# Kernel tuning notes

Hardware: AMD Instinct MI355X
Metric: run time of the kernel (lower is better)

## Reference

```python
import jax, jax.numpy as jnp
import numpy as np

N_NODES = 100000
N_EDGES = 1600000
D_IN = 128
D_HID = 128
N_CLASSES = 10
N_GRAPHS = 512


def setup_inputs() -> dict:
    key = jax.random.key(0)
    ks = jax.random.split(key, 12)
    x = jax.random.normal(ks[0], (N_NODES, D_IN), dtype=jnp.float32)
    edge_src = jax.random.randint(ks[1], (N_EDGES,), 0, N_NODES, dtype=jnp.int32)
    edge_dst = jax.random.randint(ks[2], (N_EDGES,), 0, N_NODES, dtype=jnp.int32)
    batch = jnp.sort(jax.random.randint(ks[3], (N_NODES,), 0, N_GRAPHS, dtype=jnp.int32))
    # GCNConv weights (glorot-ish scale) and biases
    def w(k, fi, fo):
        return jax.random.normal(k, (fi, fo), dtype=jnp.float32) / np.sqrt(fi)
    W0 = w(ks[4], D_IN, D_HID);  b0 = jnp.zeros((D_HID,), jnp.float32)
    W1 = w(ks[5], D_HID, D_HID); b1 = jnp.zeros((D_HID,), jnp.float32)
    W2 = w(ks[6], D_HID, D_HID); b2 = jnp.zeros((D_HID,), jnp.float32)
    Wc = w(ks[7], D_HID, N_CLASSES); bc = jnp.zeros((N_CLASSES,), jnp.float32)
    return {"x": x, "edge_src": edge_src, "edge_dst": edge_dst, "batch": batch,
            "W0": W0, "b0": b0, "W1": W1, "b1": b1, "W2": W2, "b2": b2,
            "Wc": Wc, "bc": bc}


def _gcn_conv(x, W, b, src, dst, dinv):
    # PyG GCNConv: h = x @ W; out[i] = sum_{j->i} dinv[j]*dinv[i]*h[j] (incl. self-loop) + b
    h = x @ W                                   # [N, F_out]
    norm = (dinv[src] * dinv[dst])[:, None]     # [E, 1]
    agg = jax.ops.segment_sum(h[src] * norm, dst, num_segments=N_NODES)
    agg = agg + h * (dinv * dinv)[:, None]      # self-loop contribution
    return agg + b


def reference(x, edge_src, edge_dst, batch, W0, b0, W1, b1, W2, b2, Wc, bc):
    # symmetric normalization: deg over dst with self-loops added
    deg = jax.ops.segment_sum(jnp.ones((N_EDGES,), jnp.float32), edge_dst,
                              num_segments=N_NODES) + 1.0
    dinv = jax.lax.rsqrt(deg)
    h = jax.nn.relu(_gcn_conv(x, W0, b0, edge_src, edge_dst, dinv))
    h = jax.nn.relu(_gcn_conv(h, W1, b1, edge_src, edge_dst, dinv))
    h = jax.nn.relu(_gcn_conv(h, W2, b2, edge_src, edge_dst, dinv))
    # global mean pool over graphs
    sums = jax.ops.segment_sum(h, batch, num_segments=N_GRAPHS)      # [G, D]
    cnts = jax.ops.segment_sum(jnp.ones((N_NODES,), jnp.float32), batch,
                               num_segments=N_GRAPHS)
    pooled = sums / jnp.maximum(cnts, 1.0)[:, None]
    return pooled @ Wc + bc                                          # [G, C]
```

## Files before the change

kernel.cpp:

```cpp
#include <hip/hip_runtime.h>

#define NN 100000
#define NE 1600000
#define DF 128
#define NG 512
#define NC 10
#define NBK 256
#define NPBN 391
#define BKCAP 8192
#define PCH 4096

typedef unsigned short u16;
typedef unsigned int u32;
typedef __bf16 bf16_t;
typedef bf16_t bf16x8 __attribute__((ext_vector_type(8)));
typedef float f32x4 __attribute__((ext_vector_type(4)));

__device__ __forceinline__ u16 f2bf(float f){
  u32 x=__float_as_uint(f);
  u32 r=(x+0x7fffu+((x>>16)&1u))>>16;
  return (u16)r;
}
__device__ __forceinline__ float bflo(u32 u){ return __uint_as_float(u<<16); }
__device__ __forceinline__ float bfhi(u32 u){ return __uint_as_float(u&0xffff0000u); }

__global__ void k_setup(int* __restrict__ cur,
                        const float* __restrict__ W0, const float* __restrict__ W1,
                        const float* __restrict__ W2, u16* __restrict__ WT,
                        const int* __restrict__ batch, int* __restrict__ goff){
  int i=blockIdx.x*256+threadIdx.x;
  if(i<NBK) cur[i]=0;
  if(i<3*DF*DF){
    int w=i>>14, r=i&16383;
    const float* W = (w==0)?W0:((w==1)?W1:W2);
    int k=r>>7, n=r&127;
    WT[(size_t)w*DF*DF + n*128+k]=f2bf(W[r]);
  }
  if(i<=NG){
    int lo=0, hi=NN;
    while(lo<hi){ int mid=(lo+hi)>>1; if(batch[mid]<i) lo=mid+1; else hi=mid; }
    goff[i]=lo;
  }
}

__global__ __launch_bounds__(256) void k_part(const int* __restrict__ esrc, const int* __restrict__ edst,
                                              int* __restrict__ cur, uint2* __restrict__ pairs, int n){
  __shared__ int hist[NBK], basev[NBK], lscan[NBK], lcur[NBK];
  __shared__ uint2 stage[PCH];
  int tid=threadIdx.x;
  int start=blockIdx.x*PCH, end=min(start+PCH,n);
  if(tid<NBK) hist[tid]=0;
  __syncthreads();
  for(int i=start+tid;i<end;i+=256) atomicAdd(&hist[(u32)edst[i]/NPBN],1);
  __syncthreads();
  if(tid<64){
    int carry=0;
    #pragma unroll
    for(int c=0;c<NBK;c+=64){
      int v=hist[c+tid], x=v;
      #pragma unroll
      for(int off=1;off<64;off<<=1){ int t=__shfl_up(x,off,64); if(tid>=off) x+=t; }
      lscan[c+tid]=x-v+carry;
      carry+=__shfl(x,63,64);
    }
  }
  __syncthreads();
  if(tid<NBK){ basev[tid]=atomicAdd(&cur[tid],hist[tid]); lcur[tid]=0; }
  __syncthreads();
  for(int i=start+tid;i<end;i+=256){
    int d=edst[i], s=esrc[i];
    int b=(u32)d/NPBN;
    int p=lscan[b]+atomicAdd(&lcur[b],1);
    stage[p]=make_uint2((u32)s,(u32)d);
  }
  __syncthreads();
  int ntot=end-start;
  for(int i=tid;i<ntot;i+=256){
    uint2 e=stage[i];
    int b=(u32)e.y/NPBN;
    pairs[(size_t)b*BKCAP + basev[b] + (i - lscan[b])]=e;
  }
}

__global__ __launch_bounds__(256) void k_bucket(const uint2* __restrict__ pairs, const int* __restrict__ cur,
                                                int* __restrict__ offs, float* __restrict__ dinv,
                                                int* __restrict__ csr){
  __shared__ int hist[NPBN], lsc[NPBN], curL[NBK];
  __shared__ int sbase[2];
  int b=blockIdx.x, tid=threadIdx.x;
  if(tid<NBK) curL[tid]=cur[tid];
  for(int j=tid;j<NPBN;j+=256) hist[j]=0;
  __syncthreads();
  if(tid<64){
    int acc=0;
    #pragma unroll
    for(int c=0;c<NBK;c+=64){
      int v=(c+tid<b)? curL[c+tid] : 0;
      #pragma unroll
      for(int off=32;off;off>>=1) v+=__shfl_xor(v,off,64);
      acc+=v;
    }
    if(tid==0){ sbase[0]=acc; sbase[1]=curL[b]; }
  }
  __syncthreads();
  int base=sbase[0], count=sbase[1];
  int node0=b*NPBN;
  int nnode=min(NPBN, NN-node0);
  const uint2* P=pairs+(size_t)b*BKCAP;
  for(int i=tid;i<count;i+=256) atomicAdd(&hist[P[i].y-node0],1);
  __syncthreads();
  if(tid<64){
    int carry=0;
    #pragma unroll
    for(int c=0;c<448;c+=64){
      int idx=c+tid;
      int v=(idx<NPBN)? hist[idx] : 0, x=v;
      #pragma unroll
      for(int off=1;off<64;off<<=1){ int t=__shfl_up(x,off,64); if(tid>=off) x+=t; }
      if(idx<NPBN) lsc[idx]=x-v+carry;
      carry+=__shfl(x,63,64);
    }
  }
  __syncthreads();
  for(int j=tid;j<nnode;j+=256){
    offs[node0+j]=base+lsc[j];
    dinv[node0+j]=rsqrtf((float)hist[j]+1.0f);
  }
  if(b==NBK-1 && tid==0) offs[NN]=base+count;
  __syncthreads();
  for(int j=tid;j<nnode;j+=256) hist[j]=lsc[j];
  __syncthreads();
  for(int i=tid;i<count;i+=256){
    uint2 e=P[i];
    int p=atomicAdd(&hist[e.y-node0],1);
    csr[base+p]=(int)e.x;
  }
}

template<bool F32IN>
__global__ __launch_bounds__(256) void k_gemm(const void* __restrict__ Ap, const u16* __restrict__ WT,
                                              const float* __restrict__ dinv, u16* __restrict__ outp, int n){
  __shared__ u16 sA[128][136];
  __shared__ u16 sW[128][136];
  int tid=threadIdx.x;
  int row0=blockIdx.x*128;
  {
    const uint4* p=(const uint4*)WT;
    #pragma unroll
    for(int j=0;j<8;++j){
      int c=tid+j*256;
      int r=c>>4, c8=c&15;
      *(uint4*)&sW[r][c8*8]=p[c];
    }
  }
  if(F32IN){
    const float4* A4=(const float4*)Ap;
    #pragma unroll
    for(int j=0;j<16;++j){
      int c=tid+j*256;
      int r=c>>5, c4=c&31;
      int row=row0+r;
      float4 v = (row<n)? A4[(size_t)row*32+c4] : make_float4(0.f,0.f,0.f,0.f);
      u32 lo=(u32)f2bf(v.x) | ((u32)f2bf(v.y)<<16);
      u32 hi=(u32)f2bf(v.z) | ((u32)f2bf(v.w)<<16);
      uint2 q; q.x=lo; q.y=hi;
      *(uint2*)&sA[r][c4*4]=q;
    }
  } else {
    const uint4* A4=(const uint4*)Ap;
    #pragma unroll
    for(int j=0;j<8;++j){
      int c=tid+j*256;
      int r=c>>4, c8=c&15;
      int row=row0+r;
      uint4 v = (row<n)? A4[(size_t)row*16+c8] : make_uint4(0,0,0,0);
      *(uint4*)&sA[r][c8*8]=v;
    }
  }
  __syncthreads();
  int wv=tid>>6, lane=tid&63;
  int lr=lane&15, lk=lane>>4;
  f32x4 acc[2][8];
  #pragma unroll
  for(int mr=0;mr<2;++mr)
    #pragma unroll
    for(int nt=0;nt<8;++nt) acc[mr][nt]=(f32x4){0.f,0.f,0.f,0.f};
  #pragma unroll
  for(int kk=0;kk<4;++kk){
    bf16x8 a[2], b[8];
    #pragma unroll
    for(int mr=0;mr<2;++mr)
      a[mr]=*(const bf16x8*)&sA[wv*32+mr*16+lr][kk*32+lk*8];
    #pragma unroll
    for(int nt=0;nt<8;++nt)
      b[nt]=*(const bf16x8*)&sW[nt*16+lr][kk*32+lk*8];
    #pragma unroll
    for(int mr=0;mr<2;++mr)
      #pragma unroll
      for(int nt=0;nt<8;++nt)
        acc[mr][nt]=__builtin_amdgcn_mfma_f32_16x16x32_bf16(a[mr],b[nt],acc[mr][nt],0,0,0);
  }
  #pragma unroll
  for(int mr=0;mr<2;++mr){
    int rbase=row0+wv*32+mr*16+lk*4;
    #pragma unroll
    for(int r=0;r<4;++r){
      int row=rbase+r;
      if(row<n){
        float di=dinv[row];
        #pragma unroll
        for(int nt=0;nt<8;++nt)
          outp[(size_t)row*128+nt*16+lr]=f2bf(acc[mr][nt][r]*di);
      }
    }
  }
}

__global__ __launch_bounds__(256) void k_agg(const u16* __restrict__ h2, const int* __restrict__ offs,
                                             const int* __restrict__ csr, const float* __restrict__ dinv,
                                             const float* __restrict__ bias, u16* __restrict__ outp, int n){
  int wid=threadIdx.x>>6, lane=threadIdx.x&63;
  int node=blockIdx.x*4+wid;
  if(node>=n) return;
  const u32* hv=(const u32*)h2;
  u32 sv=hv[(size_t)node*64+lane];
  float ax=bflo(sv), ay=bfhi(sv);
  int e=offs[node], e1=offs[node+1];
  for(; e+16<=e1; e+=16){
    int ii[16];
    #pragma unroll
    for(int j=0;j<16;++j) ii[j]=csr[e+j];
    u32 vv[16];
    #pragma unroll
    for(int j=0;j<16;++j) vv[j]=hv[(size_t)ii[j]*64+lane];
    #pragma unroll
    for(int j=0;j<16;++j){ ax+=bflo(vv[j]); ay+=bfhi(vv[j]); }
  }
  if(e+8<=e1){
    int ii[8];
    #pragma unroll
    for(int j=0;j<8;++j) ii[j]=csr[e+j];
    u32 vv[8];
    #pragma unroll
    for(int j=0;j<8;++j) vv[j]=hv[(size_t)ii[j]*64+lane];
    #pragma unroll
    for(int j=0;j<8;++j){ ax+=bflo(vv[j]); ay+=bfhi(vv[j]); }
    e+=8;
  }
  if(e+4<=e1){
    int i0=csr[e],i1=csr[e+1],i2=csr[e+2],i3=csr[e+3];
    u32 v0=hv[(size_t)i0*64+lane], v1=hv[(size_t)i1*64+lane];
    u32 v2=hv[(size_t)i2*64+lane], v3=hv[(size_t)i3*64+lane];
    ax+=bflo(v0)+bflo(v1)+bflo(v2)+bflo(v3);
    ay+=bfhi(v0)+bfhi(v1)+bfhi(v2)+bfhi(v3);
    e+=4;
  }
  if(e+2<=e1){
    int i0=csr[e],i1=csr[e+1];
    u32 v0=hv[(size_t)i0*64+lane], v1=hv[(size_t)i1*64+lane];
    ax+=bflo(v0)+bflo(v1);
    ay+=bfhi(v0)+bfhi(v1);
    e+=2;
  }
  if(e<e1){
    u32 v=hv[(size_t)csr[e]*64+lane];
    ax+=bflo(v); ay+=bfhi(v);
  }
  float di=dinv[node];
  float2 b=*(const float2*)&bias[lane*2];
  float ox=fmaf(di,ax,b.x), oy=fmaf(di,ay,b.y);
  ox=ox>0.f?ox:0.f; oy=oy>0.f?oy:0.f;
  u32 o=(u32)f2bf(ox) | ((u32)f2bf(oy)<<16);
  ((u32*)outp)[(size_t)node*64+lane]=o;
}

__global__ __launch_bounds__(128) void k_pool(const u16* __restrict__ h, const int* __restrict__ goff,
                                              const float* __restrict__ Wc, const float* __restrict__ bc,
                                              float* __restrict__ outp){
  __shared__ float lds[128];
  int g=blockIdx.x, d=threadIdx.x;
  int i0=goff[g], i1=goff[g+1];
  float acc=0.f;
  for(int i=i0;i<i1;++i) acc+=__uint_as_float(((u32)h[(size_t)i*128+d])<<16);
  int cnt=i1-i0;
  float p=(cnt>0)? acc/(float)cnt : 0.f;
  lds[d]=p;
  __syncthreads();
  if(d<NC){
    float s=bc[d];
    for(int k=0;k<128;++k) s=fmaf(lds[k], Wc[k*NC+d], s);
    outp[g*NC+d]=s;
  }
}

extern "C" void kernel_launch(void* const* d_in, const int* in_sizes, int n_in,
                              void* d_out, int out_size, void* d_ws, size_t ws_size,
                              hipStream_t stream){
  const float* x   =(const float*)d_in[0];
  const int* esrc  =(const int*)d_in[1];
  const int* edst  =(const int*)d_in[2];
  const int* batch =(const int*)d_in[3];
  const float* W0=(const float*)d_in[4];
  const float* b0=(const float*)d_in[5];
  const float* W1=(const float*)d_in[6];
  const float* b1=(const float*)d_in[7];
  const float* W2=(const float*)d_in[8];
  const float* b2=(const float*)d_in[9];
  const float* Wc=(const float*)d_in[10];
  const float* bc=(const float*)d_in[11];
  float* out=(float*)d_out;

  char* base=(char*)d_ws; size_t off=0;
  auto alloc=[&](size_t bytes)->void*{ off=(off+255)&~(size_t)255; void* p=base+off; off+=bytes; return p; };
  int*   cur  =(int*)  alloc(NBK*4);
  int*   offs =(int*)  alloc((size_t)(NN+1)*4);
  int*   goff =(int*)  alloc((NG+1)*4);
  float* dinv =(float*)alloc((size_t)NN*4);
  int*   csr  =(int*)  alloc((size_t)NE*4);
  uint2* pairs=(uint2*)alloc((size_t)NBK*BKCAP*8);
  u16*   WT   =(u16*)  alloc((size_t)3*DF*DF*2);
  u16*   bufA =(u16*)  alloc((size_t)NN*DF*2);
  u16*   bufB =(u16*)  alloc((size_t)NN*DF*2);
  (void)ws_size; (void)in_sizes; (void)n_in; (void)out_size;

  hipLaunchKernelGGL(k_setup,  dim3(192),  dim3(256), 0, stream, cur, W0, W1, W2, WT, batch, goff);
  hipLaunchKernelGGL(k_part,   dim3((NE+PCH-1)/PCH), dim3(256), 0, stream, esrc, edst, cur, pairs, NE);
  hipLaunchKernelGGL(k_bucket, dim3(NBK),  dim3(256), 0, stream, pairs, cur, offs, dinv, csr);

  const int GB=(NN+127)/128;
  const int AB=(NN+3)/4;

  k_gemm<true ><<<dim3(GB), dim3(256), 0, stream>>>((const void*)x,    WT,           dinv, bufA, NN);
  hipLaunchKernelGGL(k_agg,  dim3(AB), dim3(256), 0, stream, bufA, offs, csr, dinv, b0, bufB, NN);
  k_gemm<false><<<dim3(GB), dim3(256), 0, stream>>>((const void*)bufB, WT+DF*DF,     dinv, bufA, NN);
  hipLaunchKernelGGL(k_agg,  dim3(AB), dim3(256), 0, stream, bufA, offs, csr, dinv, b1, bufB, NN);
  k_gemm<false><<<dim3(GB), dim3(256), 0, stream>>>((const void*)bufB, WT+2*DF*DF,   dinv, bufA, NN);
  hipLaunchKernelGGL(k_agg,  dim3(AB), dim3(256), 0, stream, bufA, offs, csr, dinv, b2, bufB, NN);
  hipLaunchKernelGGL(k_pool, dim3(NG), dim3(128), 0, stream, bufB, goff, Wc, bc, out);
}
```

Baseline: 357.2 us.

## Fuse final aggregation with global mean pooling via LDS and global atomics

The last GCN aggregation now accumulates its ReLU outputs straight into per-graph pooled sums, using shared-memory slots and atomics, instead of writing a bf16 node buffer that a separate pool kernel reads back. A small head kernel then divides by the node counts and applies the classifier. This removes one full node-feature write and re-read, and the serial per-graph loop in the old pool kernel. In exchange it adds atomic contention and pools fp32 values where the old path pooled bf16-rounded ones.

Result: faster. 328.1 us (-8.2%).

```diff
diff --git a/kernel.cpp b/kernel.cpp
--- a/kernel.cpp
+++ b/kernel.cpp
@@ -9,6 +9,7 @@
 #define NPBN 391
 #define BKCAP 8192
 #define PCH 4096
+#define POOLSLOT 6
 
 typedef unsigned short u16;
 typedef unsigned int u32;
@@ -24,12 +25,57 @@
 __device__ __forceinline__ float bflo(u32 u){ return __uint_as_float(u<<16); }
 __device__ __forceinline__ float bfhi(u32 u){ return __uint_as_float(u&0xffff0000u); }
 
-__global__ void k_setup(int* __restrict__ cur,
+__device__ __forceinline__ void agg_node(const u32* __restrict__ hv, const int* __restrict__ csr,
+                                         int e, int e1, int lane, float& ax, float& ay){
+  for(; e+16<=e1; e+=16){
+    int ii[16];
+    #pragma unroll
+    for(int j=0;j<16;++j) ii[j]=csr[e+j];
+    u32 vv[16];
+    #pragma unroll
+    for(int j=0;j<16;++j) vv[j]=hv[(size_t)ii[j]*64+lane];
+    #pragma unroll
+    for(int j=0;j<16;++j){ ax+=bflo(vv[j]); ay+=bfhi(vv[j]); }
+  }
+  if(e+8<=e1){
+    int ii[8];
+    #pragma unroll
+    for(int j=0;j<8;++j) ii[j]=csr[e+j];
+    u32 vv[8];
+    #pragma unroll
+    for(int j=0;j<8;++j) vv[j]=hv[(size_t)ii[j]*64+lane];
+    #pragma unroll
+    for(int j=0;j<8;++j){ ax+=bflo(vv[j]); ay+=bfhi(vv[j]); }
+    e+=8;
+  }
+  if(e+4<=e1){
+    int i0=csr[e],i1=csr[e+1],i2=csr[e+2],i3=csr[e+3];
+    u32 v0=hv[(size_t)i0*64+lane], v1=hv[(size_t)i1*64+lane];
+    u32 v2=hv[(size_t)i2*64+lane], v3=hv[(size_t)i3*64+lane];
+    ax+=bflo(v0)+bflo(v1)+bflo(v2)+bflo(v3);
+    ay+=bfhi(v0)+bfhi(v1)+bfhi(v2)+bfhi(v3);
+    e+=4;
+  }
+  if(e+2<=e1){
+    int i0=csr[e],i1=csr[e+1];
+    u32 v0=hv[(size_t)i0*64+lane], v1=hv[(size_t)i1*64+lane];
+    ax+=bflo(v0)+bflo(v1);
+    ay+=bfhi(v0)+bfhi(v1);
+    e+=2;
+  }
+  if(e<e1){
+    u32 v=hv[(size_t)csr[e]*64+lane];
+    ax+=bflo(v); ay+=bfhi(v);
+  }
+}
+
+__global__ void k_setup(int* __restrict__ cur, float* __restrict__ pooled,
                         const float* __restrict__ W0, const float* __restrict__ W1,
                         const float* __restrict__ W2, u16* __restrict__ WT,
                         const int* __restrict__ batch, int* __restrict__ goff){
   int i=blockIdx.x*256+threadIdx.x;
   if(i<NBK) cur[i]=0;
+  if(i<NG*DF) pooled[i]=0.f;
   if(i<3*DF*DF){
     int w=i>>14, r=i&16383;
     const float* W = (w==0)?W0:((w==1)?W1:W2);
@@ -225,47 +271,7 @@
   const u32* hv=(const u32*)h2;
   u32 sv=hv[(size_t)node*64+lane];
   float ax=bflo(sv), ay=bfhi(sv);
-  int e=offs[node], e1=offs[node+1];
-  for(; e+16<=e1; e+=16){
-    int ii[16];
-    #pragma unroll
-    for(int j=0;j<16;++j) ii[j]=csr[e+j];
-    u32 vv[16];
-    #pragma unroll
-    for(int j=0;j<16;++j) vv[j]=hv[(size_t)ii[j]*64+lane];
-    #pragma unroll
-    for(int j=0;j<16;++j){ ax+=bflo(vv[j]); ay+=bfhi(vv[j]); }
-  }
-  if(e+8<=e1){
-    int ii[8];
-    #pragma unroll
-    for(int j=0;j<8;++j) ii[j]=csr[e+j];
-    u32 vv[8];
-    #pragma unroll
-    for(int j=0;j<8;++j) vv[j]=hv[(size_t)ii[j]*64+lane];
-    #pragma unroll
-    for(int j=0;j<8;++j){ ax+=bflo(vv[j]); ay+=bfhi(vv[j]); }
-    e+=8;
-  }
-  if(e+4<=e1){
-    int i0=csr[e],i1=csr[e+1],i2=csr[e+2],i3=csr[e+3];
-    u32 v0=hv[(size_t)i0*64+lane], v1=hv[(size_t)i1*64+lane];
-    u32 v2=hv[(size_t)i2*64+lane], v3=hv[(size_t)i3*64+lane];
-    ax+=bflo(v0)+bflo(v1)+bflo(v2)+bflo(v3);
-    ay+=bfhi(v0)+bfhi(v1)+bfhi(v2)+bfhi(v3);
-    e+=4;
-  }
-  if(e+2<=e1){
-    int i0=csr[e],i1=csr[e+1];
-    u32 v0=hv[(size_t)i0*64+lane], v1=hv[(size_t)i1*64+lane];
-    ax+=bflo(v0)+bflo(v1);
-    ay+=bfhi(v0)+bfhi(v1);
-    e+=2;
-  }
-  if(e<e1){
-    u32 v=hv[(size_t)csr[e]*64+lane];
-    ax+=bflo(v); ay+=bfhi(v);
-  }
+  agg_node(hv, csr, offs[node], offs[node+1], lane, ax, ay);
   float di=dinv[node];
   float2 b=*(const float2*)&bias[lane*2];
   float ox=fmaf(di,ax,b.x), oy=fmaf(di,ay,b.y);
@@ -274,22 +280,69 @@
   ((u32*)outp)[(size_t)node*64+lane]=o;
 }
 
-__global__ __launch_bounds__(128) void k_pool(const u16* __restrict__ h, const int* __restrict__ goff,
+__global__ __launch_bounds__(512) void k_aggpool(const u16* __restrict__ h2, const int* __restrict__ offs,
+                                                 const int* __restrict__ csr, const float* __restrict__ dinv,
+                                                 const float* __restrict__ bias, const int* __restrict__ batch,
+                                                 float* __restrict__ pooled, int n){
+  __shared__ float accL[POOLSLOT][128];
+  __shared__ int smaxL;
+  int tid=threadIdx.x, wid=tid>>6, lane=tid&63;
+  int row0=blockIdx.x*64;
+  if(tid==0) smaxL=0;
+  if(tid<128){
+    #pragma unroll
+    for(int s=0;s<POOLSLOT;++s) accL[s][tid]=0.f;
+  }
+  __syncthreads();
+  if(row0>=n) return;
+  int gbase=batch[row0];
+  const u32* hv=(const u32*)h2;
+  float2 bv=*(const float2*)&bias[lane*2];
+  int wmax=0;
+  for(int k=0;k<8;++k){
+    int node=row0+wid*8+k;
+    if(node>=n) break;
+    u32 sv=hv[(size_t)node*64+lane];
+    float ax=bflo(sv), ay=bfhi(sv);
+    agg_node(hv, csr, offs[node], offs[node+1], lane, ax, ay);
+    float di=dinv[node];
+    float ox=fmaf(di,ax,bv.x), oy=fmaf(di,ay,bv.y);
+    ox=ox>0.f?ox:0.f; oy=oy>0.f?oy:0.f;
+    int slot=batch[node]-gbase;
+    if(slot<POOLSLOT){
+      atomicAdd(&accL[slot][lane*2],  ox);
+      atomicAdd(&accL[slot][lane*2+1],oy);
+      wmax=max(wmax,slot);
+    }else{
+      atomicAdd(&pooled[(size_t)(gbase+slot)*128+lane*2],  ox);
+      atomicAdd(&pooled[(size_t)(gbase+slot)*128+lane*2+1],oy);
+    }
+  }
+  if(lane==0) atomicMax(&smaxL,wmax);
+  __syncthreads();
+  int smax=smaxL;
+  if(tid<128){
+    for(int s=0;s<=smax;++s){
+      float v=accL[s][tid];
+      if(v!=0.f) atomicAdd(&pooled[(size_t)(gbase+s)*128+tid],v);
+    }
+  }
+}
+
+__global__ __launch_bounds__(128) void k_head(const float* __restrict__ pooled, const int* __restrict__ goff,
                                               const float* __restrict__ Wc, const float* __restrict__ bc,
                                               float* __restrict__ outp){
-  __shared__ float lds[128];
+  __shared__ float pl[128];
   int g=blockIdx.x, d=threadIdx.x;
-  int i0=goff[g], i1=goff[g+1];
-  float acc=0.f;
-  for(int i=i0;i<i1;++i) acc+=__uint_as_float(((u32)h[(size_t)i*128+d])<<16);
-  int cnt=i1-i0;
-  float p=(cnt>0)? acc/(float)cnt : 0.f;
-  lds[d]=p;
+  int cnt=goff[g+1]-goff[g];
+  float s=pooled[(size_t)g*128+d];
+  pl[d]=(cnt>0)? s/(float)cnt : 0.f;
   __syncthreads();
   if(d<NC){
-    float s=bc[d];
-    for(int k=0;k<128;++k) s=fmaf(lds[k], Wc[k*NC+d], s);
-    outp[g*NC+d]=s;
+    float acc=bc[d];
+    #pragma unroll 16
+    for(int k=0;k<128;++k) acc=fmaf(pl[k], Wc[k*NC+d], acc);
+    outp[g*NC+d]=acc;
   }
 }
 
@@ -312,29 +365,31 @@
 
   char* base=(char*)d_ws; size_t off=0;
   auto alloc=[&](size_t bytes)->void*{ off=(off+255)&~(size_t)255; void* p=base+off; off+=bytes; return p; };
-  int*   cur  =(int*)  alloc(NBK*4);
-  int*   offs =(int*)  alloc((size_t)(NN+1)*4);
-  int*   goff =(int*)  alloc((NG+1)*4);
-  float* dinv =(float*)alloc((size_t)NN*4);
-  int*   csr  =(int*)  alloc((size_t)NE*4);
-  uint2* pairs=(uint2*)alloc((size_t)NBK*BKCAP*8);
-  u16*   WT   =(u16*)  alloc((size_t)3*DF*DF*2);
-  u16*   bufA =(u16*)  alloc((size_t)NN*DF*2);
-  u16*   bufB =(u16*)  alloc((size_t)NN*DF*2);
+  int*   cur   =(int*)  alloc(NBK*4);
+  int*   offs  =(int*)  alloc((size_t)(NN+1)*4);
+  int*   goff  =(int*)  alloc((NG+1)*4);
+  float* dinv  =(float*)alloc((size_t)NN*4);
+  int*   csr   =(int*)  alloc((size_t)NE*4);
+  uint2* pairs =(uint2*)alloc((size_t)NBK*BKCAP*8);
+  u16*   WT    =(u16*)  alloc((size_t)3*DF*DF*2);
+  float* pooled=(float*)alloc((size_t)NG*DF*4);
+  u16*   bufA  =(u16*)  alloc((size_t)NN*DF*2);
+  u16*   bufB  =(u16*)  alloc((size_t)NN*DF*2);
   (void)ws_size; (void)in_sizes; (void)n_in; (void)out_size;
 
-  hipLaunchKernelGGL(k_setup,  dim3(192),  dim3(256), 0, stream, cur, W0, W1, W2, WT, batch, goff);
+  hipLaunchKernelGGL(k_setup,  dim3(256),  dim3(256), 0, stream, cur, pooled, W0, W1, W2, WT, batch, goff);
   hipLaunchKernelGGL(k_part,   dim3((NE+PCH-1)/PCH), dim3(256), 0, stream, esrc, edst, cur, pairs, NE);
   hipLaunchKernelGGL(k_bucket, dim3(NBK),  dim3(256), 0, stream, pairs, cur, offs, dinv, csr);
 
   const int GB=(NN+127)/128;
   const int AB=(NN+3)/4;
-
-  k_gemm<true ><<<dim3(GB), dim3(256), 0, stream>>>((const void*)x,    WT,           dinv, bufA, NN);
+  const int PB=(NN+63)/64;
+
+  k_gemm<true ><<<dim3(GB), dim3(256), 0, stream>>>((const void*)x,    WT,         dinv, bufA, NN);
   hipLaunchKernelGGL(k_agg,  dim3(AB), dim3(256), 0, stream, bufA, offs, csr, dinv, b0, bufB, NN);
-  k_gemm<false><<<dim3(GB), dim3(256), 0, stream>>>((const void*)bufB, WT+DF*DF,     dinv, bufA, NN);
+  k_gemm<false><<<dim3(GB), dim3(256), 0, stream>>>((const void*)bufB, WT+DF*DF,   dinv, bufA, NN);
   hipLaunchKernelGGL(k_agg,  dim3(AB), dim3(256), 0, stream, bufA, offs, csr, dinv, b1, bufB, NN);
-  k_gemm<false><<<dim3(GB), dim3(256), 0, stream>>>((const void*)bufB, WT+2*DF*DF,   dinv, bufA, NN);
-  hipLaunchKernelGGL(k_agg,  dim3(AB), dim3(256), 0, stream, bufA, offs, csr, dinv, b2, bufB, NN);
-  hipLaunchKernelGGL(k_pool, dim3(NG), dim3(128), 0, stream, bufB, goff, Wc, bc, out);
-}
+  k_gemm<false><<<dim3(GB), dim3(256), 0, stream>>>((const void*)bufB, WT+2*DF*DF, dinv, bufA, NN);
+  hipLaunchKernelGGL(k_aggpool, dim3(PB), dim3(512), 0, stream, bufA, offs, csr, dinv, b2, batch, pooled, NN);
+  hipLaunchKernelGGL(k_head, dim3(NG), dim3(128), 0, stream, pooled, goff, Wc, bc, out);
+}
```
